# Kernel optimization log

Measured on AMD Instinct MI355X. Metric: run time of the kernel, lower is better.

## Reference

```python
import jax, jax.numpy as jnp
import numpy as np

N, T = 2000, 8
INFEAT, HID, OUT, H = 32, 16, 32, 4
ALPHA = 0.2
D1 = HID * H   # 64, layer-1 GRU dim (concat heads)
D2 = OUT       # 32, layer-2 GRU dim (mean heads)
NEG = -1e9


def setup_inputs() -> dict:
    key = jax.random.key(0)
    ks = jax.random.split(key, 12)
    xav = lambda k, shape, fi, fo: (jax.random.normal(k, shape, dtype=jnp.float32)
                                    * np.float32(np.sqrt(2.0 / (fi + fo))))
    # sparse-ish binary adjacency with self loops, per timestep
    A = (jax.random.uniform(ks[0], (T, N, N)) < 0.01).astype(jnp.float32)
    A = jnp.maximum(A, jnp.eye(N, dtype=jnp.float32)[None])
    feats = jax.random.normal(ks[1], (T, N, INFEAT), dtype=jnp.float32) * 0.1
    return {
        "A": A,
        "feats": feats,
        "gat1_W": xav(ks[2], (H, INFEAT, HID), INFEAT, HID),
        "gat1_a": xav(ks[3], (H, 2, HID), 2 * HID, 1),
        "gru1_W": xav(ks[4], (3, N, D1, D1), D1, D1),
        "gru1_U": xav(ks[5], (3, N, D1, D1), D1, D1),
        "gru1_b": jnp.zeros((3, N, D1), jnp.float32),
        "q1": xav(ks[6], (N, D1), N, D1),   # GAT_init_features, layer 1
        "gat2_W": xav(ks[7], (H, D1, OUT), D1, OUT),
        "gat2_a": xav(ks[8], (H, 2, OUT), 2 * OUT, 1),
        "gru2_W": xav(ks[9], (3, N, D2, D2), D2, D2),
        "gru2_U": xav(ks[10], (3, N, D2, D2), D2, D2),
        "gru2_b": jnp.zeros((3, N, D2), jnp.float32),
        "q2": xav(ks[11], (N, D2), N, D2),  # GAT_init_features, layer 2
    }


def _gat(x, At, W, a, concat):
    # x: [N,F], At: [N,N], W: [H,F,D], a: [H,2,D]
    h = jnp.einsum('nf,hfd->hnd', x, W)                       # [H,N,D]
    e_src = jnp.einsum('hnd,hd->hn', h, a[:, 0])              # [H,N]
    e_dst = jnp.einsum('hnd,hd->hn', h, a[:, 1])
    e = jax.nn.leaky_relu(e_src[:, :, None] + e_dst[:, None, :], ALPHA)
    e = jnp.where(At[None] > 0, e, NEG)
    att = jax.nn.softmax(e, axis=-1)                          # [H,N,N]
    o = jnp.einsum('hnm,hmd->hnd', att, h)
    if concat:
        return jax.nn.elu(o).transpose(1, 0, 2).reshape(x.shape[0], -1)  # [N,H*D]
    return o.mean(axis=0)                                     # [N,D]


def _gru_step(Q, Z, Wg, Ug, bg):
    # batched per-node mat_GRU_cell: Wg/Ug [3,N,D,D], bg [3,N,D]; gates: update, reset, htilda
    wz = jnp.einsum('gnij,nj->gni', Wg, Z) + bg               # [3,N,D]
    upd = jax.nn.sigmoid(wz[0] + jnp.einsum('nij,nj->ni', Ug[0], Q))
    rst = jax.nn.sigmoid(wz[1] + jnp.einsum('nij,nj->ni', Ug[1], Q))
    hcap = jnp.tanh(wz[2] + jnp.einsum('nij,nj->ni', Ug[2], rst * Q))
    return (1.0 - upd) * Q + upd * hcap


def _grcu_layer(A, feats, q0, W, a, Wg, Ug, bg, concat):
    def step(Q, inp):
        At, xt = inp
        Z = _gat(xt, At, W, a, concat)
        Qn = _gru_step(Q, Z, Wg, Ug, bg)
        return Qn, Qn
    _, seq = jax.lax.scan(step, q0, (A, feats))
    return seq  # [T,N,Dim]


def reference(A, feats, gat1_W, gat1_a, gru1_W, gru1_U, gru1_b, q1,
              gat2_W, gat2_a, gru2_W, gru2_U, gru2_b, q2):
    s1 = _grcu_layer(A, feats, q1, gat1_W, gat1_a, gru1_W, gru1_U, gru1_b, True)
    s2 = _grcu_layer(A, s1, q2, gat2_W, gat2_a, gru2_W, gru2_U, gru2_b, False)
    return s2.reshape(-1, s2.shape[-1])  # torch.cat(out_seq, dim=0) -> [T*N, OUT]
```

## Files before the change

### kernel.cpp

```cpp
#include <hip/hip_runtime.h>
#include <cstdint>
#include <cstddef>

#define NNODES 2000
#define TSTEPS 8
#define NHEADS 4
#define CAP    96
#define NROWS  (TSTEPS * NNODES)

__global__ void k1_csr_gath1(const float* __restrict__ A,
                             int* __restrict__ nbr, int* __restrict__ cnt,
                             const float* __restrict__ feats,
                             const float* __restrict__ W, const float* __restrict__ a,
                             float* __restrict__ hbuf, float* __restrict__ es,
                             float* __restrict__ ed) {
    const int lane = threadIdx.x;
    if (blockIdx.x < NROWS) {
        const int row = blockIdx.x;
        const float4* Ar4 = reinterpret_cast<const float4*>(A + (size_t)row * NNODES);
        int* outp = nbr + (size_t)row * CAP;
        const unsigned long long lmask = (1ull << lane) - 1ull;
        int c = 0;
        for (int j4 = lane; j4 < NNODES / 4; j4 += 64) {
            float4 v = Ar4[j4];
            #pragma unroll
            for (int cc = 0; cc < 4; ++cc) {
                float x = (cc == 0) ? v.x : (cc == 1) ? v.y : (cc == 2) ? v.z : v.w;
                bool p = x > 0.0f;
                unsigned long long m = __ballot(p);
                int off = __popcll(m & lmask);
                if (p && c + off < CAP) outp[c + off] = j4 * 4 + cc;
                c += (int)__popcll(m);
            }
        }
        if (lane == 0) cnt[row] = (c > CAP ? CAP : c);
    } else {
        const int b = blockIdx.x - NROWS;
        const int t = b / NNODES, n = b % NNODES;
        constexpr int F = 32, D = 16;
        const int h = lane / D, d = lane % D;
        const float* xr = feats + (size_t)b * F;
        const float* Wp = W + (size_t)h * F * D + d;
        float acc = 0.f;
        #pragma unroll
        for (int f = 0; f < F; ++f) acc += xr[f] * Wp[f * D];
        hbuf[(((size_t)t * NHEADS + h) * NNODES + n) * D + d] = acc;
        float s0 = acc * a[(h * 2 + 0) * D + d];
        float s1 = acc * a[(h * 2 + 1) * D + d];
        #pragma unroll
        for (int s = D / 2; s > 0; s >>= 1) {
            s0 += __shfl_down(s0, s, D);
            s1 += __shfl_down(s1, s, D);
        }
        if (d == 0) {
            es[((size_t)t * NHEADS + h) * NNODES + n] = s0;
            ed[((size_t)t * NHEADS + h) * NNODES + n] = s1;
        }
    }
}

template<int D, bool CONCAT>
__global__ void gat_attn_all_kernel(const int* __restrict__ nbr, const int* __restrict__ cnt_arr,
                                    const float* __restrict__ hbuf, const float* __restrict__ es,
                                    const float* __restrict__ ed, float* __restrict__ Z) {
    const int b = blockIdx.x;
    const int t = b / NNODES, n = b % NNODES;
    const int tid = threadIdx.x;
    const int h = tid / D, d = tid % D;
    const int cnt = cnt_arr[b];
    const int* idx = nbr + (size_t)b * CAP;
    const float* esb = es + (size_t)t * NHEADS * NNODES;
    const float* edb = ed + (size_t)t * NHEADS * NNODES;
    const float* hb  = hbuf + (size_t)t * NHEADS * NNODES * D;
    __shared__ int mlist[CAP];
    __shared__ float eds[NHEADS][CAP];
    for (int k = tid; k < cnt; k += NHEADS * D) mlist[k] = idx[k];
    __syncthreads();
    for (int k = d; k < cnt; k += D) eds[h][k] = edb[(size_t)h * NNODES + mlist[k]];
    __syncthreads();
    const float esv = esb[(size_t)h * NNODES + n];
    float wsum = 0.f, acc = 0.f;
    for (int k = 0; k < cnt; ++k) {
        float v = esv + eds[h][k];
        v = v > 0.f ? v : 0.2f * v;
        float w = __expf(v);
        wsum += w;
        acc += w * hb[((size_t)h * NNODES + mlist[k]) * D + d];
    }
    float o = acc / wsum;
    if constexpr (CONCAT) {
        float e = o > 0.f ? o : (__expf(o) - 1.0f);
        Z[(size_t)b * (NHEADS * D) + h * D + d] = e;
    } else {
        __shared__ float red[NHEADS][D];
        red[h][d] = o;
        __syncthreads();
        if (h == 0) Z[(size_t)b * D + d] =
            (red[0][d] + red[1][d] + red[2][d] + red[3][d]) * 0.25f;
    }
}

__global__ __launch_bounds__(256, 1)
void wzgru1_gath2_kernel(const float* __restrict__ Wg, const float* __restrict__ Ug,
                         const float* __restrict__ bg, const float* __restrict__ Z,
                         const float* __restrict__ q0,
                         const float* __restrict__ W2, const float* __restrict__ a2,
                         float* __restrict__ h2, float* __restrict__ es2,
                         float* __restrict__ ed2) {
    constexpr int D = 64;
    constexpr int TPB = 256;
    constexpr int F4R = D / 4;
    const int n = blockIdx.x, tid = threadIdx.x;
    const int quad = tid & 3;
    const int row  = tid >> 2;
    const int cbase = quad * 16;
    __shared__ float Zs[TSTEPS][D];
    __shared__ float Qh[TSTEPS][D];
    __shared__ float Qs[D], rq[D];
    __shared__ float W2s[NHEADS * 64 * 32];

    {
        const float4* W24 = reinterpret_cast<const float4*>(W2);
        float4* W2s4 = reinterpret_cast<float4*>(W2s);
        #pragma unroll
        for (int i = 0; i < 8; ++i) W2s4[i * TPB + tid] = W24[i * TPB + tid];
    }

    float wseg[3][16], useg[3][16];
    #pragma unroll
    for (int g = 0; g < 3; ++g) {
        const float4* W4 = reinterpret_cast<const float4*>(
            Wg + ((size_t)g * NNODES + n) * D * D + (size_t)row * D + cbase);
        #pragma unroll
        for (int c = 0; c < 4; ++c) {
            float4 v = W4[c];
            wseg[g][c * 4 + 0] = v.x; wseg[g][c * 4 + 1] = v.y;
            wseg[g][c * 4 + 2] = v.z; wseg[g][c * 4 + 3] = v.w;
        }
    }
    float bgv[3];
    #pragma unroll
    for (int g = 0; g < 3; ++g) bgv[g] = bg[((size_t)g * NNODES + n) * D + row];

    for (int idx = tid; idx < TSTEPS * F4R; idx += TPB) {
        int t = idx / F4R, i4 = idx % F4R;
        reinterpret_cast<float4*>(&Zs[t][0])[i4] =
            reinterpret_cast<const float4*>(Z + ((size_t)t * NNODES + n) * D)[i4];
    }
    if (tid < D) Qs[tid] = q0[(size_t)n * D + tid];
    __syncthreads();

    float wzr[3][TSTEPS];
    #pragma unroll
    for (int t = 0; t < TSTEPS; ++t) {
        float z16[16];
        #pragma unroll
        for (int c = 0; c < 4; ++c) {
            float4 v = reinterpret_cast<const float4*>(&Zs[t][cbase])[c];
            z16[c * 4 + 0] = v.x; z16[c * 4 + 1] = v.y;
            z16[c * 4 + 2] = v.z; z16[c * 4 + 3] = v.w;
        }
        #pragma unroll
        for (int g = 0; g < 3; ++g) {
            float p = 0.f;
            #pragma unroll
            for (int c = 0; c < 16; ++c) p += wseg[g][c] * z16[c];
            p += __shfl_xor(p, 1, 4); p += __shfl_xor(p, 2, 4);
            wzr[g][t] = p + bgv[g];
        }
    }

    #pragma unroll
    for (int g = 0; g < 3; ++g) {
        const float4* U4 = reinterpret_cast<const float4*>(
            Ug + ((size_t)g * NNODES + n) * D * D + (size_t)row * D + cbase);
        #pragma unroll
        for (int c = 0; c < 4; ++c) {
            float4 v = U4[c];
            useg[g][c * 4 + 0] = v.x; useg[g][c * 4 + 1] = v.y;
            useg[g][c * 4 + 2] = v.z; useg[g][c * 4 + 3] = v.w;
        }
    }

    #pragma unroll
    for (int t = 0; t < TSTEPS; ++t) {
        float q16[16];
        #pragma unroll
        for (int c = 0; c < 4; ++c) {
            float4 v = reinterpret_cast<const float4*>(&Qs[cbase])[c];
            q16[c * 4 + 0] = v.x; q16[c * 4 + 1] = v.y;
            q16[c * 4 + 2] = v.z; q16[c * 4 + 3] = v.w;
        }
        float p0 = 0.f, p1 = 0.f;
        #pragma unroll
        for (int c = 0; c < 16; ++c) { p0 += useg[0][c] * q16[c]; p1 += useg[1][c] * q16[c]; }
        p0 += __shfl_xor(p0, 1, 4); p0 += __shfl_xor(p0, 2, 4);
        p1 += __shfl_xor(p1, 1, 4); p1 += __shfl_xor(p1, 2, 4);
        const float qrow = Qs[row];
        const float zg = 1.f / (1.f + __expf(-(wzr[0][t] + p0)));
        const float rg = 1.f / (1.f + __expf(-(wzr[1][t] + p1)));
        if (quad == 0) rq[row] = rg * qrow;
        __syncthreads();
        float p2 = 0.f;
        {
            float r16[16];
            #pragma unroll
            for (int c = 0; c < 4; ++c) {
                float4 v = reinterpret_cast<const float4*>(&rq[cbase])[c];
                r16[c * 4 + 0] = v.x; r16[c * 4 + 1] = v.y;
                r16[c * 4 + 2] = v.z; r16[c * 4 + 3] = v.w;
            }
            #pragma unroll
            for (int c = 0; c < 16; ++c) p2 += useg[2][c] * r16[c];
        }
        p2 += __shfl_xor(p2, 1, 4); p2 += __shfl_xor(p2, 2, 4);
        const float hcap = tanhf(wzr[2][t] + p2);
        const float qn = (1.f - zg) * qrow + zg * hcap;
        if (quad == 0) {
            Qs[row] = qn;
            Qh[t][row] = qn;
        }
        __syncthreads();
    }

    const int lane = tid & 63;
    const int hh = tid >> 6;
    const int d2 = lane >> 1;
    const int fh = lane & 1;
    float w2seg[32];
    #pragma unroll
    for (int j = 0; j < 32; ++j)
        w2seg[j] = W2s[((size_t)(hh * 64 + fh * 32 + j)) * 32 + d2];
    const float a0 = a2[(hh * 2 + 0) * 32 + d2];
    const float a1 = a2[(hh * 2 + 1) * 32 + d2];
    #pragma unroll
    for (int t = 0; t < TSTEPS; ++t) {
        float q32[32];
        #pragma unroll
        for (int c = 0; c < 8; ++c) {
            float4 v = reinterpret_cast<const float4*>(&Qh[t][fh * 32])[c];
            q32[c * 4 + 0] = v.x; q32[c * 4 + 1] = v.y;
            q32[c * 4 + 2] = v.z; q32[c * 4 + 3] = v.w;
        }
        float p = 0.f;
        #pragma unroll
        for (int j = 0; j < 32; ++j) p += w2seg[j] * q32[j];
        p += __shfl_xor(p, 1, 64);
        if (fh == 0) h2[(((size_t)t * NHEADS + hh) * NNODES + n) * 32 + d2] = p;
        float e0 = (fh == 0) ? p * a0 : 0.f;
        float e1 = (fh == 0) ? p * a1 : 0.f;
        #pragma unroll
        for (int s = 2; s <= 32; s <<= 1) {
            e0 += __shfl_xor(e0, s, 64);
            e1 += __shfl_xor(e1, s, 64);
        }
        if (lane == 0) {
            es2[((size_t)t * NHEADS + hh) * NNODES + n] = e0;
            ed2[((size_t)t * NHEADS + hh) * NNODES + n] = e1;
        }
    }
}

__global__ __launch_bounds__(64, 1)
void wzgru2_kernel(const float* __restrict__ Wg, const float* __restrict__ Ug,
                   const float* __restrict__ bg, const float* __restrict__ Z,
                   const float* __restrict__ q0, float* __restrict__ outp) {
    constexpr int D = 32;
    constexpr int TPB = 64;
    constexpr int F4R = D / 4;
    const int n = blockIdx.x, tid = threadIdx.x;
    const int quad = tid & 1;
    const int row  = tid >> 1;
    const int cbase = quad * 16;
    __shared__ float Zs[TSTEPS][D];
    __shared__ float Qs[D], rq[D];

    float wseg[3][16], useg[3][16];
    #pragma unroll
    for (int g = 0; g < 3; ++g) {
        const float4* W4 = reinterpret_cast<const float4*>(
            Wg + ((size_t)g * NNODES + n) * D * D + (size_t)row * D + cbase);
        #pragma unroll
        for (int c = 0; c < 4; ++c) {
            float4 v = W4[c];
            wseg[g][c * 4 + 0] = v.x; wseg[g][c * 4 + 1] = v.y;
            wseg[g][c * 4 + 2] = v.z; wseg[g][c * 4 + 3] = v.w;
        }
    }
    #pragma unroll
    for (int g = 0; g < 3; ++g) {
        const float4* U4 = reinterpret_cast<const float4*>(
            Ug + ((size_t)g * NNODES + n) * D * D + (size_t)row * D + cbase);
        #pragma unroll
        for (int c = 0; c < 4; ++c) {
            float4 v = U4[c];
            useg[g][c * 4 + 0] = v.x; useg[g][c * 4 + 1] = v.y;
            useg[g][c * 4 + 2] = v.z; useg[g][c * 4 + 3] = v.w;
        }
    }
    float bgv[3];
    #pragma unroll
    for (int g = 0; g < 3; ++g) bgv[g] = bg[((size_t)g * NNODES + n) * D + row];

    for (int idx = tid; idx < TSTEPS * F4R; idx += TPB) {
        int t = idx / F4R, i4 = idx % F4R;
        reinterpret_cast<float4*>(&Zs[t][0])[i4] =
            reinterpret_cast<const float4*>(Z + ((size_t)t * NNODES + n) * D)[i4];
    }
    if (tid < D) Qs[tid] = q0[(size_t)n * D + tid];
    __syncthreads();

    float wzr[3][TSTEPS];
    #pragma unroll
    for (int t = 0; t < TSTEPS; ++t) {
        float z16[16];
        #pragma unroll
        for (int c = 0; c < 4; ++c) {
            float4 v = reinterpret_cast<const float4*>(&Zs[t][cbase])[c];
            z16[c * 4 + 0] = v.x; z16[c * 4 + 1] = v.y;
            z16[c * 4 + 2] = v.z; z16[c * 4 + 3] = v.w;
        }
        #pragma unroll
        for (int g = 0; g < 3; ++g) {
            float p = 0.f;
            #pragma unroll
            for (int c = 0; c < 16; ++c) p += wseg[g][c] * z16[c];
            p += __shfl_xor(p, 1, 2);
            wzr[g][t] = p + bgv[g];
        }
    }

    #pragma unroll
    for (int t = 0; t < TSTEPS; ++t) {
        float q16[16];
        #pragma unroll
        for (int c = 0; c < 4; ++c) {
            float4 v = reinterpret_cast<const float4*>(&Qs[cbase])[c];
            q16[c * 4 + 0] = v.x; q16[c * 4 + 1] = v.y;
            q16[c * 4 + 2] = v.z; q16[c * 4 + 3] = v.w;
        }
        float p0 = 0.f, p1 = 0.f;
        #pragma unroll
        for (int c = 0; c < 16; ++c) { p0 += useg[0][c] * q16[c]; p1 += useg[1][c] * q16[c]; }
        p0 += __shfl_xor(p0, 1, 2);
        p1 += __shfl_xor(p1, 1, 2);
        const float qrow = Qs[row];
        const float zg = 1.f / (1.f + __expf(-(wzr[0][t] + p0)));
        const float rg = 1.f / (1.f + __expf(-(wzr[1][t] + p1)));
        if (quad == 0) rq[row] = rg * qrow;
        __syncthreads();
        float p2 = 0.f;
        {
            float r16[16];
            #pragma unroll
            for (int c = 0; c < 4; ++c) {
                float4 v = reinterpret_cast<const float4*>(&rq[cbase])[c];
                r16[c * 4 + 0] = v.x; r16[c * 4 + 1] = v.y;
                r16[c * 4 + 2] = v.z; r16[c * 4 + 3] = v.w;
            }
            #pragma unroll
            for (int c = 0; c < 16; ++c) p2 += useg[2][c] * r16[c];
        }
        p2 += __shfl_xor(p2, 1, 2);
        const float hcap = tanhf(wzr[2][t] + p2);
        const float qn = (1.f - zg) * qrow + zg * hcap;
        if (quad == 0) {
            Qs[row] = qn;
            outp[((size_t)t * NNODES + n) * D + row] = qn;
        }
        __syncthreads();
    }
}

extern "C" void kernel_launch(void* const* d_in, const int* in_sizes, int n_in,
                              void* d_out, int out_size, void* d_ws, size_t ws_size,
                              hipStream_t stream) {
    const float* A      = (const float*)d_in[0];
    const float* feats  = (const float*)d_in[1];
    const float* gat1_W = (const float*)d_in[2];
    const float* gat1_a = (const float*)d_in[3];
    const float* gru1_W = (const float*)d_in[4];
    const float* gru1_U = (const float*)d_in[5];
    const float* gru1_b = (const float*)d_in[6];
    const float* q1     = (const float*)d_in[7];
    const float* gat2_W = (const float*)d_in[8];
    const float* gat2_a = (const float*)d_in[9];
    const float* gru2_W = (const float*)d_in[10];
    const float* gru2_U = (const float*)d_in[11];
    const float* gru2_b = (const float*)d_in[12];
    const float* q2     = (const float*)d_in[13];
    float* out = (float*)d_out;

    char* ws = (char*)d_ws;
    int*   nbr  = (int*)ws;    ws += (size_t)NROWS * CAP * 4;
    int*   cnt  = (int*)ws;    ws += (size_t)NROWS * 4;
    float* h1   = (float*)ws;  ws += (size_t)TSTEPS * NHEADS * NNODES * 16 * 4;
    float* es1  = (float*)ws;  ws += (size_t)TSTEPS * NHEADS * NNODES * 4;
    float* ed1  = (float*)ws;  ws += (size_t)TSTEPS * NHEADS * NNODES * 4;
    float* Z1   = (float*)ws;  ws += (size_t)TSTEPS * NNODES * 64 * 4;
    float* h2   = (float*)ws;  ws += (size_t)TSTEPS * NHEADS * NNODES * 32 * 4;
    float* es2  = (float*)ws;  ws += (size_t)TSTEPS * NHEADS * NNODES * 4;
    float* ed2  = (float*)ws;  ws += (size_t)TSTEPS * NHEADS * NNODES * 4;
    float* Z2   = (float*)ws;  ws += (size_t)TSTEPS * NNODES * 32 * 4;

    k1_csr_gath1<<<2 * NROWS, 64, 0, stream>>>(A, nbr, cnt, feats, gat1_W, gat1_a,
                                               h1, es1, ed1);
    gat_attn_all_kernel<16, true><<<NROWS, 64, 0, stream>>>(nbr, cnt, h1, es1, ed1, Z1);
    wzgru1_gath2_kernel<<<NNODES, 256, 0, stream>>>(gru1_W, gru1_U, gru1_b, Z1, q1,
                                                    gat2_W, gat2_a, h2, es2, ed2);
    gat_attn_all_kernel<32, false><<<NROWS, 128, 0, stream>>>(nbr, cnt, h2, es2, ed2, Z2);
    wzgru2_kernel<<<NNODES, 64, 0, stream>>>(gru2_W, gru2_U, gru2_b, Z2, q2, out);
}
```

Before: 150.3 us.

## Stage GRU U weights in LDS, reuse buffer for W2, precompute attention exps

In the layer-1 GRU kernel, U gate weights are now staged in shared memory and reloaded each timestep instead of held in registers, and W weights are loaded one gate at a time. This lowers register pressure. The W2 shared buffer is aliased onto the U staging area after the recurrence, which cuts the peak LDS footprint. In the attention kernel, the leaky-relu and exp of each edge score are computed once per neighbor while the scores are gathered, rather than inside the accumulation loop. The cost is extra LDS traffic every timestep and one added barrier.

New measurement: 165.2 us. 1.1x slower.

```diff
diff --git a/kernel.cpp b/kernel.cpp
--- a/kernel.cpp
+++ b/kernel.cpp
@@ -76,14 +76,16 @@
     __shared__ float eds[NHEADS][CAP];
     for (int k = tid; k < cnt; k += NHEADS * D) mlist[k] = idx[k];
     __syncthreads();
-    for (int k = d; k < cnt; k += D) eds[h][k] = edb[(size_t)h * NNODES + mlist[k]];
+    const float esv = esb[(size_t)h * NNODES + n];
+    for (int k = d; k < cnt; k += D) {
+        float v = esv + edb[(size_t)h * NNODES + mlist[k]];
+        v = v > 0.f ? v : 0.2f * v;
+        eds[h][k] = __expf(v);
+    }
     __syncthreads();
-    const float esv = esb[(size_t)h * NNODES + n];
     float wsum = 0.f, acc = 0.f;
     for (int k = 0; k < cnt; ++k) {
-        float v = esv + eds[h][k];
-        v = v > 0.f ? v : 0.2f * v;
-        float w = __expf(v);
+        float w = eds[h][k];
         wsum += w;
         acc += w * hb[((size_t)h * NNODES + mlist[k]) * D + d];
     }
@@ -117,68 +119,57 @@
     __shared__ float Zs[TSTEPS][D];
     __shared__ float Qh[TSTEPS][D];
     __shared__ float Qs[D], rq[D];
-    __shared__ float W2s[NHEADS * 64 * 32];
-
-    {
-        const float4* W24 = reinterpret_cast<const float4*>(W2);
-        float4* W2s4 = reinterpret_cast<float4*>(W2s);
-        #pragma unroll
-        for (int i = 0; i < 8; ++i) W2s4[i * TPB + tid] = W24[i * TPB + tid];
-    }
-
-    float wseg[3][16], useg[3][16];
+    __shared__ float4 u4[3][4][TPB];
+
+    float4 ureg[3][4];
     #pragma unroll
     for (int g = 0; g < 3; ++g) {
-        const float4* W4 = reinterpret_cast<const float4*>(
-            Wg + ((size_t)g * NNODES + n) * D * D + (size_t)row * D + cbase);
-        #pragma unroll
-        for (int c = 0; c < 4; ++c) {
-            float4 v = W4[c];
-            wseg[g][c * 4 + 0] = v.x; wseg[g][c * 4 + 1] = v.y;
-            wseg[g][c * 4 + 2] = v.z; wseg[g][c * 4 + 3] = v.w;
-        }
-    }
-    float bgv[3];
-    #pragma unroll
-    for (int g = 0; g < 3; ++g) bgv[g] = bg[((size_t)g * NNODES + n) * D + row];
-
+        const float4* U4 = reinterpret_cast<const float4*>(
+            Ug + ((size_t)g * NNODES + n) * D * D + (size_t)row * D + cbase);
+        #pragma unroll
+        for (int c = 0; c < 4; ++c) ureg[g][c] = U4[c];
+    }
     for (int idx = tid; idx < TSTEPS * F4R; idx += TPB) {
         int t = idx / F4R, i4 = idx % F4R;
         reinterpret_cast<float4*>(&Zs[t][0])[i4] =
             reinterpret_cast<const float4*>(Z + ((size_t)t * NNODES + n) * D)[i4];
     }
     if (tid < D) Qs[tid] = q0[(size_t)n * D + tid];
+    float bgv[3];
+    #pragma unroll
+    for (int g = 0; g < 3; ++g) bgv[g] = bg[((size_t)g * NNODES + n) * D + row];
+    #pragma unroll
+    for (int g = 0; g < 3; ++g)
+        #pragma unroll
+        for (int c = 0; c < 4; ++c) u4[g][c][tid] = ureg[g][c];
     __syncthreads();
 
     float wzr[3][TSTEPS];
     #pragma unroll
-    for (int t = 0; t < TSTEPS; ++t) {
-        float z16[16];
-        #pragma unroll
-        for (int c = 0; c < 4; ++c) {
-            float4 v = reinterpret_cast<const float4*>(&Zs[t][cbase])[c];
-            z16[c * 4 + 0] = v.x; z16[c * 4 + 1] = v.y;
-            z16[c * 4 + 2] = v.z; z16[c * 4 + 3] = v.w;
-        }
-        #pragma unroll
-        for (int g = 0; g < 3; ++g) {
+    for (int g = 0; g < 3; ++g) {
+        float wseg[16];
+        const float4* W4 = reinterpret_cast<const float4*>(
+            Wg + ((size_t)g * NNODES + n) * D * D + (size_t)row * D + cbase);
+        #pragma unroll
+        for (int c = 0; c < 4; ++c) {
+            float4 v = W4[c];
+            wseg[c * 4 + 0] = v.x; wseg[c * 4 + 1] = v.y;
+            wseg[c * 4 + 2] = v.z; wseg[c * 4 + 3] = v.w;
+        }
+        #pragma unroll
+        for (int t = 0; t < TSTEPS; ++t) {
+            float z16[16];
+            #pragma unroll
+            for (int c = 0; c < 4; ++c) {
+                float4 v = reinterpret_cast<const float4*>(&Zs[t][cbase])[c];
+                z16[c * 4 + 0] = v.x; z16[c * 4 + 1] = v.y;
+                z16[c * 4 + 2] = v.z; z16[c * 4 + 3] = v.w;
+            }
             float p = 0.f;
             #pragma unroll
-            for (int c = 0; c < 16; ++c) p += wseg[g][c] * z16[c];
+            for (int c = 0; c < 16; ++c) p += wseg[c] * z16[c];
             p += __shfl_xor(p, 1, 4); p += __shfl_xor(p, 2, 4);
             wzr[g][t] = p + bgv[g];
-        }
-    }
-
-    #pragma unroll
-    for (int g = 0; g < 3; ++g) {
-        const float4* U4 = reinterpret_cast<const float4*>(
-            Ug + ((size_t)g * NNODES + n) * D * D + (size_t)row * D + cbase);
-        #pragma unroll
-        for (int c = 0; c < 4; ++c) {
-            float4 v = U4[c];
-            useg[g][c * 4 + 0] = v.x; useg[g][c * 4 + 1] = v.y;
-            useg[g][c * 4 + 2] = v.z; useg[g][c * 4 + 3] = v.w;
         }
     }
 
@@ -191,9 +182,19 @@
             q16[c * 4 + 0] = v.x; q16[c * 4 + 1] = v.y;
             q16[c * 4 + 2] = v.z; q16[c * 4 + 3] = v.w;
         }
+        float u0v[16], u1v[16];
+        #pragma unroll
+        for (int cc = 0; cc < 4; ++cc) {
+            float4 a = u4[0][cc][tid];
+            u0v[cc * 4 + 0] = a.x; u0v[cc * 4 + 1] = a.y;
+            u0v[cc * 4 + 2] = a.z; u0v[cc * 4 + 3] = a.w;
+            float4 b = u4[1][cc][tid];
+            u1v[cc * 4 + 0] = b.x; u1v[cc * 4 + 1] = b.y;
+            u1v[cc * 4 + 2] = b.z; u1v[cc * 4 + 3] = b.w;
+        }
         float p0 = 0.f, p1 = 0.f;
         #pragma unroll
-        for (int c = 0; c < 16; ++c) { p0 += useg[0][c] * q16[c]; p1 += useg[1][c] * q16[c]; }
+        for (int c = 0; c < 16; ++c) { p0 += u0v[c] * q16[c]; p1 += u1v[c] * q16[c]; }
         p0 += __shfl_xor(p0, 1, 4); p0 += __shfl_xor(p0, 2, 4);
         p1 += __shfl_xor(p1, 1, 4); p1 += __shfl_xor(p1, 2, 4);
         const float qrow = Qs[row];
@@ -203,15 +204,18 @@
         __syncthreads();
         float p2 = 0.f;
         {
-            float r16[16];
+            float r16[16], u2v[16];
             #pragma unroll
             for (int c = 0; c < 4; ++c) {
                 float4 v = reinterpret_cast<const float4*>(&rq[cbase])[c];
                 r16[c * 4 + 0] = v.x; r16[c * 4 + 1] = v.y;
                 r16[c * 4 + 2] = v.z; r16[c * 4 + 3] = v.w;
+                float4 u = u4[2][c][tid];
+                u2v[c * 4 + 0] = u.x; u2v[c * 4 + 1] = u.y;
+                u2v[c * 4 + 2] = u.z; u2v[c * 4 + 3] = u.w;
             }
             #pragma unroll
-            for (int c = 0; c < 16; ++c) p2 += useg[2][c] * r16[c];
+            for (int c = 0; c < 16; ++c) p2 += u2v[c] * r16[c];
         }
         p2 += __shfl_xor(p2, 1, 4); p2 += __shfl_xor(p2, 2, 4);
         const float hcap = tanhf(wzr[2][t] + p2);
@@ -222,6 +226,15 @@
         }
         __syncthreads();
     }
+
+    float* W2s = reinterpret_cast<float*>(&u4[0][0][0]);
+    {
+        const float4* W24 = reinterpret_cast<const float4*>(W2);
+        float4* W2s4 = reinterpret_cast<float4*>(W2s);
+        #pragma unroll
+        for (int i = 0; i < 8; ++i) W2s4[i * TPB + tid] = W24[i * TPB + tid];
+    }
+    __syncthreads();
 
     const int lane = tid & 63;
     const int hh = tid >> 6;
```
